# Optimization experiments

Measured on AMD Instinct MI355X. Metric: run time of the kernel, lower is better.

Reference implementation:

```python
import jax, jax.numpy as jnp
import numpy as np

D = 64  # hidden_dim


def _bn(x, gamma, beta):
    # eval-mode BatchNorm1d with running_mean=0, running_var=1 (fresh model)
    return gamma * x + beta


def _edge_conv(h, W, b, gamma, beta):
    # h: [B,N,D]; W: [2D,D] split into Wi (acts on x_i) and Wj (acts on x_j)
    Wi, Wj = W[:D], W[D:]
    ti = jnp.einsum('bnd,de->bne', h, Wi)  # [B,N,D] (i term)
    tj = jnp.einsum('bmd,de->bme', h, Wj)  # [B,N,D] (j term)
    # e[b,i,j,:] = x_i@Wi + x_j@Wj + b  -> relu -> BN -> max over j
    e = ti[:, :, None, :] + tj[:, None, :, :] + b  # [B,N,N,D]
    e = _bn(jax.nn.relu(e), gamma, beta)
    return e.max(axis=2)  # [B,N,D]


def setup_inputs() -> dict:
    key = jax.random.key(0)
    ks = jax.random.split(key, 16)
    s = lambda k, shp, sc: (jax.random.normal(k, shp, dtype=jnp.float32) * sc)
    inp = {
        'x': s(ks[0], (32, 256, 4), 1.0),
        'W1': s(ks[1], (4, D), 0.5), 'b1': s(ks[2], (D,), 0.1),
        'g1': 1.0 + s(ks[3], (D,), 0.1), 'beta1': s(ks[4], (D,), 0.1),
        'We1': s(ks[5], (2 * D, D), 0.1), 'be1': s(ks[6], (D,), 0.1),
        'ge1': 1.0 + s(ks[7], (D,), 0.1), 'betae1': s(ks[8], (D,), 0.1),
        'We2': s(ks[9], (2 * D, D), 0.1), 'be2': s(ks[10], (D,), 0.1),
        'ge2': 1.0 + s(ks[11], (D,), 0.1), 'betae2': s(ks[12], (D,), 0.1),
        'Wg1': s(ks[13], (2 * D, D), 0.1), 'bg1': s(ks[14], (D,), 0.1),
        'Wg2': s(ks[15], (D, 2), 0.1), 'bg2': jnp.zeros((2,), jnp.float32),
    }
    return inp


def reference(x, W1, b1, g1, beta1, We1, be1, ge1, betae1, We2, be2, ge2, betae2, Wg1, bg1, Wg2, bg2):
    # input MLP: Linear -> ReLU -> BN (eval)
    h = _bn(jax.nn.relu(x @ W1 + b1), g1, beta1)  # [B,N,D]
    h = _edge_conv(h, We1, be1, ge1, betae1)
    h = _edge_conv(h, We2, be2, ge2, betae2)
    x_mean = h.mean(axis=1)  # [B,D]
    x_max = h.max(axis=1)    # [B,D]
    xg = jnp.concatenate([x_mean, x_max], axis=-1)  # [B,2D]
    # global MLP (dropout is identity in eval)
    out = jax.nn.relu(xg @ Wg1 + bg1) @ Wg2 + bg2  # [B,2]
    return out
```

## Files before the change

kernel.cpp:

```cpp
#include <hip/hip_runtime.h>

#define NB 32
#define NN 256
#define DD 64
#define SROW 68
#define TPAD 17
#define FMAXV 3.402823466e+38f


__device__ __forceinline__ void conv_full(
    const float* Hs, int n, int d0, const float* __restrict__ We,
    float ti[16], float tj[16])
{
#pragma unroll
    for (int j = 0; j < 16; ++j) { ti[j] = 0.f; tj[j] = 0.f; }
    const float* hrow = Hs + (size_t)n * SROW;
#pragma unroll 1
    for (int kc = 0; kc < 4; ++kc) {
        float h[16];
#pragma unroll
        for (int q = 0; q < 4; ++q) {
            float4 hv = *(const float4*)(hrow + kc * 16 + 4 * q);
            h[4*q+0] = hv.x; h[4*q+1] = hv.y; h[4*q+2] = hv.z; h[4*q+3] = hv.w;
        }
#pragma unroll
        for (int q = 0; q < 16; ++q) asm volatile("" : "+v"(h[q]));
#pragma unroll
        for (int kk = 0; kk < 16; ++kk) {
            const float hk = h[kk];
            const float* wi = We + (size_t)(kc * 16 + kk) * DD + d0;
            const float* wj = We + (size_t)(DD + kc * 16 + kk) * DD + d0;
#pragma unroll
            for (int q = 0; q < 4; ++q) {
                float4 a = *(const float4*)(wi + 4 * q);
                float4 c = *(const float4*)(wj + 4 * q);
                ti[4*q+0] = fmaf(hk, a.x, ti[4*q+0]);
                ti[4*q+1] = fmaf(hk, a.y, ti[4*q+1]);
                ti[4*q+2] = fmaf(hk, a.z, ti[4*q+2]);
                ti[4*q+3] = fmaf(hk, a.w, ti[4*q+3]);
                tj[4*q+0] = fmaf(hk, c.x, tj[4*q+0]);
                tj[4*q+1] = fmaf(hk, c.y, tj[4*q+1]);
                tj[4*q+2] = fmaf(hk, c.z, tj[4*q+2]);
                tj[4*q+3] = fmaf(hk, c.w, tj[4*q+3]);
            }
        }
    }
}

__global__ __launch_bounds__(1024, 4) void k_all(
    const float* __restrict__ x,
    const float* __restrict__ W1,  const float* __restrict__ b1,
    const float* __restrict__ g1,  const float* __restrict__ beta1,
    const float* __restrict__ We1, const float* __restrict__ be1,
    const float* __restrict__ ge1, const float* __restrict__ bte1,
    const float* __restrict__ We2, const float* __restrict__ be2,
    const float* __restrict__ ge2, const float* __restrict__ bte2,
    const float* __restrict__ Wg1, const float* __restrict__ bg1,
    const float* __restrict__ Wg2, const float* __restrict__ bg2,
    float* __restrict__ out)
{
    __shared__ __align__(16) float Hs[NN * SROW];
    __shared__ __align__(16) float PTmax[4][DD], PTmin[4][DD];
    __shared__ __align__(16) float RM[DD], RMn[DD];
    __shared__ __align__(16) float PS[4][DD], PM[4][DD];
    __shared__ __align__(16) float xg[2 * DD];
    __shared__ __align__(16) float hid[DD];

    const int b   = blockIdx.x;
    const int l   = threadIdx.x & 63;
    const int w   = __builtin_amdgcn_readfirstlane(threadIdx.x >> 6);
    const int ng  = w >> 2;
    const int d0  = (w & 3) * 16;
    const int n   = ng * 64 + l;
    const int jd  = l >> 2;
    const int cq  = l & 3;
    float* Ts     = Hs + w * (64 * TPAD);

    {
        float4 xv = *(const float4*)(x + ((size_t)b * NN + n) * 4);
#pragma unroll
        for (int q = 0; q < 4; ++q) {
            float hq[4];
#pragma unroll
            for (int u = 0; u < 4; ++u) {
                const int d = d0 + 4 * q + u;
                float a = b1[d];
                a = fmaf(xv.x, W1[0 * DD + d], a);
                a = fmaf(xv.y, W1[1 * DD + d], a);
                a = fmaf(xv.z, W1[2 * DD + d], a);
                a = fmaf(xv.w, W1[3 * DD + d], a);
                hq[u] = g1[d] * fmaxf(a, 0.f) + beta1[d];
            }
            *(float4*)(Hs + (size_t)n * SROW + d0 + 4 * q) =
                make_float4(hq[0], hq[1], hq[2], hq[3]);
        }
    }
    __syncthreads();

    float ti[16], tj[16];

    conv_full(Hs, n, d0, We1, ti, tj);
    __syncthreads();

#pragma unroll
    for (int j = 0; j < 16; ++j) Ts[l * TPAD + j] = tj[j];
    __syncthreads();

    {
        float mx = -FMAXV, mn = FMAXV;
#pragma unroll
        for (int r = 0; r < 16; ++r) {
            float v = Ts[(cq * 16 + r) * TPAD + jd];
            mx = fmaxf(mx, v); mn = fminf(mn, v);
        }
        mx = fmaxf(mx, __shfl_xor(mx, 1, 64));
        mx = fmaxf(mx, __shfl_xor(mx, 2, 64));
        mn = fminf(mn, __shfl_xor(mn, 1, 64));
        mn = fminf(mn, __shfl_xor(mn, 2, 64));
        if (cq == 0) { PTmax[ng][d0 + jd] = mx; PTmin[ng][d0 + jd] = mn; }
    }
    __syncthreads();

    {
        const int t = threadIdx.x;
        if (t < DD)
            RM[t] = fmaxf(fmaxf(PTmax[0][t], PTmax[1][t]),
                          fmaxf(PTmax[2][t], PTmax[3][t]));
        else if (t < 2 * DD) {
            const int d = t - DD;
            RMn[d] = fminf(fminf(PTmin[0][d], PTmin[1][d]),
                           fminf(PTmin[2][d], PTmin[3][d]));
        }
    }
    __syncthreads();

    {
#pragma unroll
        for (int q = 0; q < 4; ++q) {
            float4 rmx = *(const float4*)(&RM[d0 + 4 * q]);
            float4 rmn = *(const float4*)(&RMn[d0 + 4 * q]);
            const float rmax[4] = {rmx.x, rmx.y, rmx.z, rmx.w};
            const float rmin[4] = {rmn.x, rmn.y, rmn.z, rmn.w};
            float hq[4];
#pragma unroll
            for (int u = 0; u < 4; ++u) {
                const int d = d0 + 4 * q + u;
                const float gv = ge1[d];
                const float sv = ti[4*q+u] + (gv >= 0.f ? rmax[u] : rmin[u]) + be1[d];
                hq[u] = gv * fmaxf(sv, 0.f) + bte1[d];
            }
            *(float4*)(Hs + (size_t)n * SROW + d0 + 4 * q) =
                make_float4(hq[0], hq[1], hq[2], hq[3]);
        }
    }
    __syncthreads();

    conv_full(Hs, n, d0, We2, ti, tj);
    __syncthreads();

#pragma unroll
    for (int j = 0; j < 16; ++j) Ts[l * TPAD + j] = tj[j];
    __syncthreads();

    {
        float mx = -FMAXV, mn = FMAXV;
#pragma unroll
        for (int r = 0; r < 16; ++r) {
            float v = Ts[(cq * 16 + r) * TPAD + jd];
            mx = fmaxf(mx, v); mn = fminf(mn, v);
        }
        mx = fmaxf(mx, __shfl_xor(mx, 1, 64));
        mx = fmaxf(mx, __shfl_xor(mx, 2, 64));
        mn = fminf(mn, __shfl_xor(mn, 1, 64));
        mn = fminf(mn, __shfl_xor(mn, 2, 64));
        if (cq == 0) { PTmax[ng][d0 + jd] = mx; PTmin[ng][d0 + jd] = mn; }
    }
    __syncthreads();

    {
        const int t = threadIdx.x;
        if (t < DD)
            RM[t] = fmaxf(fmaxf(PTmax[0][t], PTmax[1][t]),
                          fmaxf(PTmax[2][t], PTmax[3][t]));
        else if (t < 2 * DD) {
            const int d = t - DD;
            RMn[d] = fminf(fminf(PTmin[0][d], PTmin[1][d]),
                           fminf(PTmin[2][d], PTmin[3][d]));
        }
    }
    __syncthreads();

    {
#pragma unroll
        for (int q = 0; q < 4; ++q) {
            float4 rmx = *(const float4*)(&RM[d0 + 4 * q]);
            float4 rmn = *(const float4*)(&RMn[d0 + 4 * q]);
            const float rmax[4] = {rmx.x, rmx.y, rmx.z, rmx.w};
            const float rmin[4] = {rmn.x, rmn.y, rmn.z, rmn.w};
#pragma unroll
            for (int u = 0; u < 4; ++u) {
                const int d = d0 + 4 * q + u;
                const float gv = ge2[d];
                const float sv = ti[4*q+u] + (gv >= 0.f ? rmax[u] : rmin[u]) + be2[d];
                Ts[l * TPAD + 4 * q + u] = gv * fmaxf(sv, 0.f) + bte2[d];
            }
        }
    }
    __syncthreads();

    {
        float s = 0.f, mx = -FMAXV;
#pragma unroll
        for (int r = 0; r < 16; ++r) {
            float v = Ts[(cq * 16 + r) * TPAD + jd];
            s += v; mx = fmaxf(mx, v);
        }
        s += __shfl_xor(s, 1, 64);
        s += __shfl_xor(s, 2, 64);
        mx = fmaxf(mx, __shfl_xor(mx, 1, 64));
        mx = fmaxf(mx, __shfl_xor(mx, 2, 64));
        if (cq == 0) { PS[ng][d0 + jd] = s; PM[ng][d0 + jd] = mx; }
    }
    __syncthreads();

    const int t = threadIdx.x;
    if (t < DD) {
        xg[t] = (PS[0][t] + PS[1][t] + PS[2][t] + PS[3][t]) * (1.f / 256.f);
    } else if (t < 2 * DD) {
        const int d = t - DD;
        xg[t] = fmaxf(fmaxf(PM[0][d], PM[1][d]), fmaxf(PM[2][d], PM[3][d]));
    }
    __syncthreads();
    if (t < DD) {
        float a = bg1[t];
#pragma unroll
        for (int k = 0; k < 2 * DD; ++k) a = fmaf(xg[k], Wg1[k * DD + t], a);
        hid[t] = fmaxf(a, 0.f);
    }
    __syncthreads();
    if (t < 2) {
        float o = bg2[t];
#pragma unroll
        for (int j = 0; j < DD; ++j) o = fmaf(hid[j], Wg2[j * 2 + t], o);
        out[b * 2 + t] = o;
    }
}

extern "C" void kernel_launch(void* const* d_in, const int* in_sizes, int n_in,
                              void* d_out, int out_size, void* d_ws, size_t ws_size,
                              hipStream_t stream) {
    const float* x     = (const float*)d_in[0];
    const float* W1    = (const float*)d_in[1];
    const float* b1    = (const float*)d_in[2];
    const float* g1    = (const float*)d_in[3];
    const float* beta1 = (const float*)d_in[4];
    const float* We1   = (const float*)d_in[5];
    const float* be1   = (const float*)d_in[6];
    const float* ge1   = (const float*)d_in[7];
    const float* bte1  = (const float*)d_in[8];
    const float* We2   = (const float*)d_in[9];
    const float* be2   = (const float*)d_in[10];
    const float* ge2   = (const float*)d_in[11];
    const float* bte2  = (const float*)d_in[12];
    const float* Wg1   = (const float*)d_in[13];
    const float* bg1   = (const float*)d_in[14];
    const float* Wg2   = (const float*)d_in[15];
    const float* bg2   = (const float*)d_in[16];

    k_all<<<dim3(NB), dim3(1024), 0, stream>>>(
        x, W1, b1, g1, beta1,
        We1, be1, ge1, bte1,
        We2, be2, ge2, bte2,
        Wg1, bg1, Wg2, bg2, (float*)d_out);
}
```

Measured before the change: 120.6 us.

## Split first edge-conv into separate wide-grid kernel before fused remainder

Moves the input MLP and first edge-conv projection into a new kernel launched over 256 blocks (8 per batch), each computing a slice of features for 64 points. It writes ti to a workspace and per-group partial max/min of tj, which the second kernel reduces before continuing with the second conv and global MLP. The goal is to spread the first conv across more compute units than the original 32 blocks. The cost is an extra launch and a global-memory round trip for the ti buffer.

```diff
diff --git a/kernel.cpp b/kernel.cpp
--- a/kernel.cpp
+++ b/kernel.cpp
@@ -7,6 +7,73 @@
 #define TPAD 17
 #define FMAXV 3.402823466e+38f
 
+
+__global__ __launch_bounds__(512, 2) void k1_conv(
+    const float* __restrict__ x,
+    const float* __restrict__ W1,  const float* __restrict__ b1,
+    const float* __restrict__ g1,  const float* __restrict__ beta1,
+    const float* __restrict__ We1,
+    float* __restrict__ TI, float* __restrict__ PMAX, float* __restrict__ PMIN)
+{
+    const int blk = blockIdx.x;
+    const int b   = blk >> 3;
+    const int g   = (blk >> 1) & 3;
+    const int dh  = blk & 1;
+    const int l   = threadIdx.x & 63;
+    const int w   = __builtin_amdgcn_readfirstlane(threadIdx.x >> 6);
+    const int n   = g * 64 + l;
+    const int d0  = dh * 32 + w * 4;
+
+    float h[DD];
+    {
+        float4 xv = *(const float4*)(x + ((size_t)b * NN + n) * 4);
+#pragma unroll
+        for (int j = 0; j < DD; ++j) {
+            float a = b1[j];
+            a = fmaf(xv.x, W1[0 * DD + j], a);
+            a = fmaf(xv.y, W1[1 * DD + j], a);
+            a = fmaf(xv.z, W1[2 * DD + j], a);
+            a = fmaf(xv.w, W1[3 * DD + j], a);
+            h[j] = g1[j] * fmaxf(a, 0.f) + beta1[j];
+        }
+    }
+
+    float ti[4] = {0.f, 0.f, 0.f, 0.f}, tj[4] = {0.f, 0.f, 0.f, 0.f};
+#pragma unroll
+    for (int k = 0; k < DD; ++k) {
+        const float* wi = We1 + k * DD + d0;
+        const float* wj = We1 + (DD + k) * DD + d0;
+#pragma unroll
+        for (int j = 0; j < 4; ++j) {
+            ti[j] = fmaf(h[k], wi[j], ti[j]);
+            tj[j] = fmaf(h[k], wj[j], tj[j]);
+        }
+    }
+    *(float4*)(TI + ((size_t)(b * NN + n)) * DD + d0) =
+        make_float4(ti[0], ti[1], ti[2], ti[3]);
+
+    float mx[4], mn[4];
+#pragma unroll
+    for (int j = 0; j < 4; ++j) { mx[j] = tj[j]; mn[j] = tj[j]; }
+#pragma unroll
+    for (int m = 1; m < 64; m <<= 1) {
+#pragma unroll
+        for (int j = 0; j < 4; ++j) {
+            mx[j] = fmaxf(mx[j], __shfl_xor(mx[j], m, 64));
+            mn[j] = fminf(mn[j], __shfl_xor(mn[j], m, 64));
+        }
+    }
+    float smx = mx[0], smn = mn[0];
+#pragma unroll
+    for (int j = 1; j < 4; ++j) {
+        smx = (l == j) ? mx[j] : smx;
+        smn = (l == j) ? mn[j] : smn;
+    }
+    if (l < 4) {
+        PMAX[(b * 4 + g) * DD + d0 + l] = smx;
+        PMIN[(b * 4 + g) * DD + d0 + l] = smn;
+    }
+}
 
 __device__ __forceinline__ void conv_full(
     const float* Hs, int n, int d0, const float* __restrict__ We,
@@ -47,14 +114,13 @@
     }
 }
 
-__global__ __launch_bounds__(1024, 4) void k_all(
-    const float* __restrict__ x,
-    const float* __restrict__ W1,  const float* __restrict__ b1,
-    const float* __restrict__ g1,  const float* __restrict__ beta1,
-    const float* __restrict__ We1, const float* __restrict__ be1,
-    const float* __restrict__ ge1, const float* __restrict__ bte1,
-    const float* __restrict__ We2, const float* __restrict__ be2,
-    const float* __restrict__ ge2, const float* __restrict__ bte2,
+__global__ __launch_bounds__(1024, 4) void k2_rest(
+    const float* __restrict__ PMAXin, const float* __restrict__ PMINin,
+    const float* __restrict__ be1P, const float* __restrict__ ge1P,
+    const float* __restrict__ bte1P,
+    const float* __restrict__ We2, const float* __restrict__ TIin,
+    const float* __restrict__ be2P, const float* __restrict__ ge2P,
+    const float* __restrict__ bte2P,
     const float* __restrict__ Wg1, const float* __restrict__ bg1,
     const float* __restrict__ Wg2, const float* __restrict__ bg2,
     float* __restrict__ out)
@@ -77,19 +143,39 @@
     float* Ts     = Hs + w * (64 * TPAD);
 
     {
-        float4 xv = *(const float4*)(x + ((size_t)b * NN + n) * 4);
+        float rmx[16], rmn[16];
 #pragma unroll
         for (int q = 0; q < 4; ++q) {
+            const int dq = d0 + 4 * q;
+            float4 a0 = *(const float4*)(PMAXin + (b * 4 + 0) * DD + dq);
+            float4 a1 = *(const float4*)(PMAXin + (b * 4 + 1) * DD + dq);
+            float4 a2 = *(const float4*)(PMAXin + (b * 4 + 2) * DD + dq);
+            float4 a3 = *(const float4*)(PMAXin + (b * 4 + 3) * DD + dq);
+            rmx[4*q+0] = fmaxf(fmaxf(a0.x, a1.x), fmaxf(a2.x, a3.x));
+            rmx[4*q+1] = fmaxf(fmaxf(a0.y, a1.y), fmaxf(a2.y, a3.y));
+            rmx[4*q+2] = fmaxf(fmaxf(a0.z, a1.z), fmaxf(a2.z, a3.z));
+            rmx[4*q+3] = fmaxf(fmaxf(a0.w, a1.w), fmaxf(a2.w, a3.w));
+            float4 i0 = *(const float4*)(PMINin + (b * 4 + 0) * DD + dq);
+            float4 i1 = *(const float4*)(PMINin + (b * 4 + 1) * DD + dq);
+            float4 i2 = *(const float4*)(PMINin + (b * 4 + 2) * DD + dq);
+            float4 i3 = *(const float4*)(PMINin + (b * 4 + 3) * DD + dq);
+            rmn[4*q+0] = fminf(fminf(i0.x, i1.x), fminf(i2.x, i3.x));
+            rmn[4*q+1] = fminf(fminf(i0.y, i1.y), fminf(i2.y, i3.y));
+            rmn[4*q+2] = fminf(fminf(i0.z, i1.z), fminf(i2.z, i3.z));
+            rmn[4*q+3] = fminf(fminf(i0.w, i1.w), fminf(i2.w, i3.w));
+        }
+        const float* tip = TIin + ((size_t)(b * NN + n)) * DD + d0;
+#pragma unroll
+        for (int q = 0; q < 4; ++q) {
+            float4 t = *(const float4*)(tip + 4 * q);
+            const float tv[4] = {t.x, t.y, t.z, t.w};
             float hq[4];
 #pragma unroll
             for (int u = 0; u < 4; ++u) {
                 const int d = d0 + 4 * q + u;
-                float a = b1[d];
-                a = fmaf(xv.x, W1[0 * DD + d], a);
-                a = fmaf(xv.y, W1[1 * DD + d], a);
-                a = fmaf(xv.z, W1[2 * DD + d], a);
-                a = fmaf(xv.w, W1[3 * DD + d], a);
-                hq[u] = g1[d] * fmaxf(a, 0.f) + beta1[d];
+                const float gv = ge1P[d];
+                const float sv = tv[u] + (gv >= 0.f ? rmx[4*q+u] : rmn[4*q+u]) + be1P[d];
+                hq[u] = gv * fmaxf(sv, 0.f) + bte1P[d];
             }
             *(float4*)(Hs + (size_t)n * SROW + d0 + 4 * q) =
                 make_float4(hq[0], hq[1], hq[2], hq[3]);
@@ -98,8 +184,7 @@
     __syncthreads();
 
     float ti[16], tj[16];
-
-    conv_full(Hs, n, d0, We1, ti, tj);
+    conv_full(Hs, n, d0, We2, ti, tj);
     __syncthreads();
 
 #pragma unroll
@@ -137,72 +222,16 @@
     {
 #pragma unroll
         for (int q = 0; q < 4; ++q) {
-            float4 rmx = *(const float4*)(&RM[d0 + 4 * q]);
-            float4 rmn = *(const float4*)(&RMn[d0 + 4 * q]);
-            const float rmax[4] = {rmx.x, rmx.y, rmx.z, rmx.w};
-            const float rmin[4] = {rmn.x, rmn.y, rmn.z, rmn.w};
-            float hq[4];
+            float4 rmx4 = *(const float4*)(&RM[d0 + 4 * q]);
+            float4 rmn4 = *(const float4*)(&RMn[d0 + 4 * q]);
+            const float rmax[4] = {rmx4.x, rmx4.y, rmx4.z, rmx4.w};
+            const float rmin[4] = {rmn4.x, rmn4.y, rmn4.z, rmn4.w};
 #pragma unroll
             for (int u = 0; u < 4; ++u) {
                 const int d = d0 + 4 * q + u;
-                const float gv = ge1[d];
-                const float sv = ti[4*q+u] + (gv >= 0.f ? rmax[u] : rmin[u]) + be1[d];
-                hq[u] = gv * fmaxf(sv, 0.f) + bte1[d];
-            }
-            *(float4*)(Hs + (size_t)n * SROW + d0 + 4 * q) =
-                make_float4(hq[0], hq[1], hq[2], hq[3]);
-        }
-    }
-    __syncthreads();
-
-    conv_full(Hs, n, d0, We2, ti, tj);
-    __syncthreads();
-
-#pragma unroll
-    for (int j = 0; j < 16; ++j) Ts[l * TPAD + j] = tj[j];
-    __syncthreads();
-
-    {
-        float mx = -FMAXV, mn = FMAXV;
-#pragma unroll
-        for (int r = 0; r < 16; ++r) {
-            float v = Ts[(cq * 16 + r) * TPAD + jd];
-            mx = fmaxf(mx, v); mn = fminf(mn, v);
-        }
-        mx = fmaxf(mx, __shfl_xor(mx, 1, 64));
-        mx = fmaxf(mx, __shfl_xor(mx, 2, 64));
-        mn = fminf(mn, __shfl_xor(mn, 1, 64));
-        mn = fminf(mn, __shfl_xor(mn, 2, 64));
-        if (cq == 0) { PTmax[ng][d0 + jd] = mx; PTmin[ng][d0 + jd] = mn; }
-    }
-    __syncthreads();
-
-    {
-        const int t = threadIdx.x;
-        if (t < DD)
-            RM[t] = fmaxf(fmaxf(PTmax[0][t], PTmax[1][t]),
-                          fmaxf(PTmax[2][t], PTmax[3][t]));
-        else if (t < 2 * DD) {
-            const int d = t - DD;
-            RMn[d] = fminf(fminf(PTmin[0][d], PTmin[1][d]),
-                           fminf(PTmin[2][d], PTmin[3][d]));
-        }
-    }
-    __syncthreads();
-
-    {
-#pragma unroll
-        for (int q = 0; q < 4; ++q) {
-            float4 rmx = *(const float4*)(&RM[d0 + 4 * q]);
-            float4 rmn = *(const float4*)(&RMn[d0 + 4 * q]);
-            const float rmax[4] = {rmx.x, rmx.y, rmx.z, rmx.w};
-            const float rmin[4] = {rmn.x, rmn.y, rmn.z, rmn.w};
-#pragma unroll
-            for (int u = 0; u < 4; ++u) {
-                const int d = d0 + 4 * q + u;
-                const float gv = ge2[d];
-                const float sv = ti[4*q+u] + (gv >= 0.f ? rmax[u] : rmin[u]) + be2[d];
-                Ts[l * TPAD + 4 * q + u] = gv * fmaxf(sv, 0.f) + bte2[d];
+                const float gv = ge2P[d];
+                const float sv = ti[4*q+u] + (gv >= 0.f ? rmax[u] : rmin[u]) + be2P[d];
+                Ts[l * TPAD + 4 * q + u] = gv * fmaxf(sv, 0.f) + bte2P[d];
             }
         }
     }
@@ -267,9 +296,14 @@
     const float* Wg2   = (const float*)d_in[15];
     const float* bg2   = (const float*)d_in[16];
 
-    k_all<<<dim3(NB), dim3(1024), 0, stream>>>(
-        x, W1, b1, g1, beta1,
-        We1, be1, ge1, bte1,
-        We2, be2, ge2, bte2,
-        Wg1, bg1, Wg2, bg2, (float*)d_out);
+    float* ws    = (float*)d_ws;
+    float* TI1   = ws;
+    float* PMAX1 = ws + 524288;
+    float* PMIN1 = ws + 532480;
+
+    k1_conv<<<dim3(NB * 8), dim3(512), 0, stream>>>(
+        x, W1, b1, g1, beta1, We1, TI1, PMAX1, PMIN1);
+    k2_rest<<<dim3(NB), dim3(1024), 0, stream>>>(
+        PMAX1, PMIN1, be1, ge1, bte1, We2, TI1,
+        be2, ge2, bte2, Wg1, bg1, Wg2, bg2, (float*)d_out);
 }
```

Result: no change. 120.4 us (-0.1%).
